# Performance work log

Hardware: AMD Instinct MI355X
Metric: run time of the kernel (lower is better)

The kernel has to match this reference:

```python
import jax, jax.numpy as jnp
import numpy as np

N_USER, N_ITEM, D, N_LAYER, NNZ, B = 50000, 100000, 64, 3, 2400000, 4096
NEG_SLOPE = 0.2
EPS = 1e-12


def setup_inputs() -> dict:
    key = jax.random.key(0)
    ks = jax.random.split(key, 12)
    N = N_USER + N_ITEM
    user_emb = jax.random.normal(ks[0], (N_USER, D), dtype=jnp.float32) * 0.1
    item_emb = jax.random.normal(ks[1], (N_ITEM, D), dtype=jnp.float32) * 0.1
    rows = jax.random.randint(ks[2], (NNZ,), 0, N, dtype=jnp.int32)
    cols = jax.random.randint(ks[3], (NNZ,), 0, N, dtype=jnp.int32)
    edge_index = jnp.stack([rows, cols])  # [2, nnz] COO indices of sparse L
    # normalized-Laplacian-like positive values, ~1/deg scale
    edge_vals = jax.random.uniform(ks[4], (NNZ,), dtype=jnp.float32) * (1.0 / 16.0)
    scale = 1.0 / np.sqrt(D)
    W1 = jax.random.normal(ks[5], (N_LAYER, D, D), dtype=jnp.float32) * scale
    W2 = jax.random.normal(ks[6], (N_LAYER, D, D), dtype=jnp.float32) * scale
    b1 = jnp.zeros((N_LAYER, D), dtype=jnp.float32)
    b2 = jnp.zeros((N_LAYER, D), dtype=jnp.float32)
    users = jax.random.randint(ks[7], (B,), 1, N_USER + 1, dtype=jnp.int32)      # 1-indexed
    pos_items = jax.random.randint(ks[8], (B,), 1, N_ITEM + 1, dtype=jnp.int32)  # 1-indexed
    neg_items = jax.random.randint(ks[9], (B,), 1, N_ITEM + 1, dtype=jnp.int32)  # 1-indexed
    return {"user_emb": user_emb, "item_emb": item_emb, "edge_vals": edge_vals,
            "W1": W1, "b1": b1, "W2": W2, "b2": b2,
            "edge_index": edge_index, "users": users,
            "pos_items": pos_items, "neg_items": neg_items}


def _spmm(rows, cols, vals, E, num_nodes):
    # sparse COO L @ E : gather source rows, scale by edge value, scatter-add to dest rows
    return jax.ops.segment_sum(vals[:, None] * E[cols], rows, num_segments=num_nodes)


def reference(user_emb, item_emb, edge_vals, W1, b1, W2, b2,
              edge_index, users, pos_items, neg_items):
    n_user = user_emb.shape[0]
    N = n_user + item_emb.shape[0]
    rows, cols = edge_index[0], edge_index[1]
    E = jnp.concatenate([user_emb, item_emb], axis=0)  # [N, d]
    all_E = [E]
    for i in range(W1.shape[0]):
        LE = _spmm(rows, cols, edge_vals, E, N)          # L @ E
        # (L + I) @ E @ W1 + (L@E * E) @ W2  (dropouts are eval-mode identity)
        h = (LE + E) @ W1[i] + b1[i] + (LE * E) @ W2[i] + b2[i]
        E = jax.nn.leaky_relu(h, NEG_SLOPE)
        nrm = jnp.maximum(jnp.linalg.norm(E, axis=1, keepdims=True), EPS)
        all_E.append(E / nrm)  # L2-normalized copy stored; unnormalized E propagates
    all_E = jnp.concatenate(all_E, axis=1)               # [N, d*(1+L)]
    u_emb = all_E[:n_user][users - 1]
    items = all_E[n_user:]
    return u_emb, items[pos_items - 1], items[neg_items - 1]
```

## Files before the change

### kernel.cpp

```cpp
#include <hip/hip_runtime.h>

#define N_USERC 50000
#define N_ITEMC 100000
#define NN      150000
#define DD      64
#define NLAYER  3
#define NNZC    2400000
#define BB      4096
#define NRID    (3*BB)
#define NBKT    147
#define NABLK   586
#define NTILE   4688
#define ELLW    32
#define ELLROWS 150528
#define OVCAP   32768

typedef unsigned short ushort_t;
typedef __attribute__((ext_vector_type(8))) short bf16x8;
typedef __attribute__((ext_vector_type(4))) float f32x4;

static __device__ __forceinline__ float bf2f(ushort_t b) {
    unsigned int u = ((unsigned int)b) << 16;
    return __uint_as_float(u);
}
static __device__ __forceinline__ ushort_t f2bf(float f) {
    unsigned int u = __float_as_uint(f);
    u = u + 0x7FFFu + ((u >> 16) & 1u);
    return (ushort_t)(u >> 16);
}

__global__ __launch_bounds__(256) void k_sniffzb(const unsigned int* __restrict__ ue_words,
                                                 int* __restrict__ flag,
                                                 int* __restrict__ bucket_cnt,
                                                 int* __restrict__ ovcnt) {
    int t = threadIdx.x;
    if (t < 64) {
        int cnt = 0;
        for (int i = 0; i < 4; i++) {
            unsigned int w = ue_words[t * 4 + i];
            unsigned int lo = w & 0xFFFFu;
            unsigned int ex = (lo >> 7) & 0xFF;
            if (ex >= 100 && ex <= 132) cnt++;
        }
        for (int m = 1; m < 64; m <<= 1) cnt += __shfl_xor(cnt, m, 64);
        if (t == 0) *flag = (cnt >= 128) ? 1 : 0;
    } else if (t - 64 < NBKT) {
        bucket_cnt[t - 64] = 0;
    } else if (t == 255) {
        *ovcnt = 0;
    }
}

__global__ __launch_bounds__(256) void k_initb(const void* __restrict__ ue,
                                               const void* __restrict__ ie,
                                               const int* __restrict__ flag,
                                               ushort_t* __restrict__ Eb0) {
    int i4 = blockIdx.x * 256 + threadIdx.x;
    if (i4 >= NN * DD / 4) return;
    int idx = i4 * 4;
    int row = idx >> 6;
    bool isU = row < N_USERC;
    int si = isU ? idx : idx - N_USERC * DD;
    if (*flag) {
        const uint2* src = (const uint2*)((const ushort_t*)(isU ? ue : ie) + si);
        *(uint2*)(Eb0 + idx) = *src;
    } else {
        const float* src = (const float*)(isU ? ue : ie) + si;
        ushort_t o[4];
#pragma unroll
        for (int k = 0; k < 4; k++) o[k] = f2bf(src[k]);
        *(uint2*)(Eb0 + idx) = *(uint2*)o;
    }
}

__global__ __launch_bounds__(256) void k_wprep(const void* __restrict__ W1,
                                               const void* __restrict__ W2,
                                               const void* __restrict__ b1,
                                               const void* __restrict__ b2,
                                               const int* __restrict__ flag,
                                               ushort_t* __restrict__ Wfrag,
                                               float* __restrict__ bsum) {
    int idx = blockIdx.x * 256 + threadIdx.x;
    int isbf = *flag;
    if (idx < NLAYER * 4 * 4 * 64 * 8) {
        int i    = idx & 7;
        int lane = (idx >> 3) & 63;
        int jt   = (idx >> 9) & 3;
        int s    = (idx >> 11) & 3;
        int l    = idx >> 13;
        int kfull = 32 * (s & 1) + 8 * (lane >> 4) + i;
        int col   = jt * 16 + (lane & 15);
        const void* W = (s < 2) ? W1 : W2;
        size_t off = (size_t)l * 4096 + (size_t)kfull * 64 + col;
        float v = isbf ? bf2f(((const ushort_t*)W)[off]) : ((const float*)W)[off];
        Wfrag[idx] = f2bf(v);
    } else {
        int r = idx - NLAYER * 4 * 4 * 64 * 8;
        if (r < NLAYER * 64) {
            float v1 = isbf ? bf2f(((const ushort_t*)b1)[r]) : ((const float*)b1)[r];
            float v2 = isbf ? bf2f(((const ushort_t*)b2)[r]) : ((const float*)b2)[r];
            bsum[r] = v1 + v2;
        }
    }
}

__global__ __launch_bounds__(256) void k_bhist(const int* __restrict__ rows,
                                               int* __restrict__ bucket_cnt) {
    __shared__ int h[NBKT];
    int t = threadIdx.x;
    if (t < NBKT) h[t] = 0;
    __syncthreads();
    int e0 = blockIdx.x * 4096;
#pragma unroll
    for (int i = 0; i < 16; i++) {
        int e = e0 + t + i * 256;
        if (e < NNZC) atomicAdd(&h[rows[e] >> 10], 1);
    }
    __syncthreads();
    if (t < NBKT && h[t]) atomicAdd(&bucket_cnt[t], h[t]);
}

__global__ __launch_bounds__(256) void k_bscan(const int* __restrict__ bucket_cnt,
                                               int* __restrict__ gbase,
                                               int* __restrict__ gcursor) {
    __shared__ int s[256];
    int t = threadIdx.x;
    int v = (t < NBKT) ? bucket_cnt[t] : 0;
    s[t] = v; __syncthreads();
    for (int off = 1; off < 256; off <<= 1) {
        int x = (t >= off) ? s[t - off] : 0;
        __syncthreads();
        s[t] += x;
        __syncthreads();
    }
    if (t < NBKT) { int ex = s[t] - v; gbase[t] = ex; gcursor[t] = ex; }
    if (t == 0) { gbase[NBKT] = NNZC; }
}

__global__ __launch_bounds__(256) void k_phaseA(const int* __restrict__ rows,
                                                const int* __restrict__ cols,
                                                const void* __restrict__ vals,
                                                const int* __restrict__ flag,
                                                int* __restrict__ gcursor,
                                                int2* __restrict__ binned) {
    __shared__ int hist[NBKT], base_[NBKT], lcur[NBKT];
    int t = threadIdx.x;
    int e0 = blockIdx.x * 4096;
    if (t < NBKT) { hist[t] = 0; lcur[t] = 0; }
    __syncthreads();
    int myrow[16];
#pragma unroll
    for (int i = 0; i < 16; i++) {
        int e = e0 + t + i * 256;
        int r = -1;
        if (e < NNZC) { r = rows[e]; atomicAdd(&hist[r >> 10], 1); }
        myrow[i] = r;
    }
    __syncthreads();
    if (t < NBKT && hist[t] > 0) base_[t] = atomicAdd(&gcursor[t], hist[t]);
    __syncthreads();
    int isbf = *flag;
#pragma unroll
    for (int i = 0; i < 16; i++) {
        int e = e0 + t + i * 256;
        if (e < NNZC) {
            int r = myrow[i];
            int bkt = r >> 10;
            int off = atomicAdd(&lcur[bkt], 1);
            int pos = base_[bkt] + off;
            int c = cols[e];
            float v = isbf ? bf2f(((const ushort_t*)vals)[e]) : ((const float*)vals)[e];
            binned[pos] = make_int2(((r & 1023) << 18) | c, __float_as_int(v));
        }
    }
}

__global__ __launch_bounds__(256) void k_phaseB(const int* __restrict__ gbase,
                                                const int2* __restrict__ binned,
                                                int2* __restrict__ ell,
                                                int4* __restrict__ ovbuf,
                                                int* __restrict__ ovcnt) {
    __shared__ int rcur[1024];
    int b = blockIdx.x, t = threadIdx.x;
    int s = gbase[b], e = gbase[b + 1];
    for (int i = t; i < 1024; i += 256) rcur[i] = 0;
    __syncthreads();
    for (int i = s + t; i < e; i += 256) {
        int2 en = binned[i];
        int rl = en.x >> 18;
        int c  = en.x & 0x3FFFF;
        int off = atomicAdd(&rcur[rl], 1);
        if (off < ELLW) {
            ell[((size_t)(b * 1024 + rl)) * ELLW + off] = make_int2(c, en.y);
        } else {
            int p = atomicAdd(ovcnt, 1);
            if (p < OVCAP) ovbuf[p] = make_int4(b * 1024 + rl, c, en.y, 0);
        }
    }
    __syncthreads();
    for (int i = t; i < 1024; i += 256) {
        int start = rcur[i]; if (start > ELLW) start = ELLW;
        int2* rp = ell + ((size_t)(b * 1024 + i)) * ELLW;
        for (int j = start; j < ELLW; j++) rp[j] = make_int2(0, 0);
    }
}

__global__ __launch_bounds__(256) void k_layer(const int2* __restrict__ ell,
                                               const int4* __restrict__ ovbuf,
                                               const int* __restrict__ ovcnt,
                                               const ushort_t* __restrict__ Eb_in,
                                               ushort_t* __restrict__ Eb_out,
                                               const ushort_t* __restrict__ Wfrag,
                                               const float* __restrict__ bsum,
                                               int layer) {
    __shared__ float sLE[32][68];
    __shared__ float sE [32][68];

    int t    = threadIdx.x;
    int wv   = t >> 6;
    int lane = t & 63;
    int oct  = lane >> 3;
    int d8   = (lane & 7) * 8;
    int hl   = lane >> 4;
    int l16  = lane & 15;
    int r0   = blockIdx.x << 5;

    int lr_ = t >> 3;
    int dm_ = (t & 7) * 8;
    uint4 ev = make_uint4(0u, 0u, 0u, 0u);
    {
        int gr = r0 + lr_;
        if (gr < NN) ev = *(const uint4*)(Eb_in + (size_t)gr * DD + dm_);
    }

    int baseRow = r0 + wv * 8;
    int2 pv_c[4], pv_n[4];
    uint4 q_c[4];
#pragma unroll
    for (int v = 0; v < 4; v++)
        pv_c[v] = ell[(size_t)baseRow * ELLW + v * 8 + oct];
#pragma unroll
    for (int v = 0; v < 4; v++)
        q_c[v] = *(const uint4*)(Eb_in + ((size_t)(unsigned)pv_c[v].x << 6) + d8);
#pragma unroll
    for (int v = 0; v < 4; v++)
        pv_n[v] = ell[(size_t)(baseRow + 1) * ELLW + v * 8 + oct];

#pragma unroll
    for (int sub = 0; sub < 8; sub++) {
        uint4 q_n[4];
        int2 pv_n2[4];
        if (sub < 7) {
#pragma unroll
            for (int v = 0; v < 4; v++)
                q_n[v] = *(const uint4*)(Eb_in + ((size_t)(unsigned)pv_n[v].x << 6) + d8);
        }
        if (sub < 6) {
#pragma unroll
            for (int v = 0; v < 4; v++)
                pv_n2[v] = ell[(size_t)(baseRow + sub + 2) * ELLW + v * 8 + oct];
        }
        float acc[8];
#pragma unroll
        for (int k = 0; k < 8; k++) acc[k] = 0.f;
#pragma unroll
        for (int v = 0; v < 4; v++) {
            float w = __int_as_float(pv_c[v].y);
            acc[0] = fmaf(w, __uint_as_float(q_c[v].x << 16),         acc[0]);
            acc[1] = fmaf(w, __uint_as_float(q_c[v].x & 0xffff0000u), acc[1]);
            acc[2] = fmaf(w, __uint_as_float(q_c[v].y << 16),         acc[2]);
            acc[3] = fmaf(w, __uint_as_float(q_c[v].y & 0xffff0000u), acc[3]);
            acc[4] = fmaf(w, __uint_as_float(q_c[v].z << 16),         acc[4]);
            acc[5] = fmaf(w, __uint_as_float(q_c[v].z & 0xffff0000u), acc[5]);
            acc[6] = fmaf(w, __uint_as_float(q_c[v].w << 16),         acc[6]);
            acc[7] = fmaf(w, __uint_as_float(q_c[v].w & 0xffff0000u), acc[7]);
        }
#pragma unroll
        for (int m = 8; m < 64; m <<= 1)
#pragma unroll
            for (int k = 0; k < 8; k++) acc[k] += __shfl_xor(acc[k], m, 64);
        if (oct == 0) {
            int lr = wv * 8 + sub;
            *(float4*)&sLE[lr][d8]     = make_float4(acc[0], acc[1], acc[2], acc[3]);
            *(float4*)&sLE[lr][d8 + 4] = make_float4(acc[4], acc[5], acc[6], acc[7]);
        }
#pragma unroll
        for (int v = 0; v < 4; v++) {
            pv_c[v] = pv_n[v];
            q_c[v]  = q_n[v];
            pv_n[v] = pv_n2[v];
        }
    }

    sE[lr_][dm_ + 0] = __uint_as_float(ev.x << 16);
    sE[lr_][dm_ + 1] = __uint_as_float(ev.x & 0xffff0000u);
    sE[lr_][dm_ + 2] = __uint_as_float(ev.y << 16);
    sE[lr_][dm_ + 3] = __uint_as_float(ev.y & 0xffff0000u);
    sE[lr_][dm_ + 4] = __uint_as_float(ev.z << 16);
    sE[lr_][dm_ + 5] = __uint_as_float(ev.z & 0xffff0000u);
    sE[lr_][dm_ + 6] = __uint_as_float(ev.w << 16);
    sE[lr_][dm_ + 7] = __uint_as_float(ev.w & 0xffff0000u);
    __syncthreads();

    {
        int n = *ovcnt;
        n = (n < OVCAP) ? n : OVCAP;
        if (wv == 0) {
            for (int i = 0; i < n; i++) {
                int4 ov = ovbuf[i];
                if ((unsigned)(ov.x - r0) < 32u) {
                    float w = __int_as_float(ov.z);
                    sLE[ov.x - r0][lane] += w * bf2f(Eb_in[(size_t)ov.y * DD + lane]);
                }
            }
        }
    }
    __syncthreads();

    int rt = wv & 1;
    int j0w = wv >> 1;
    int jtA = 2 * j0w, jtB = 2 * j0w + 1;
    const uint4* wb = (const uint4*)(Wfrag + (size_t)layer * 8192);
    float bsA = bsum[layer * 64 + jtA * 16 + l16];
    float bsB = bsum[layer * 64 + jtB * 16 + l16];

    f32x4 accA = (f32x4){0.f, 0.f, 0.f, 0.f};
    f32x4 accB = (f32x4){0.f, 0.f, 0.f, 0.f};
    int lrow = rt * 16 + l16;

#pragma unroll
    for (int sh = 0; sh < 2; sh++) {
        bf16x8 w1a, w1b, w2a, w2b;
        {
            uint4 qa = wb[(sh * 4 + jtA) * 64 + lane];
            uint4 qb = wb[(sh * 4 + jtB) * 64 + lane];
            uint4 qc = wb[((2 + sh) * 4 + jtA) * 64 + lane];
            uint4 qd = wb[((2 + sh) * 4 + jtB) * 64 + lane];
            __builtin_memcpy(&w1a, &qa, 16);
            __builtin_memcpy(&w1b, &qb, 16);
            __builtin_memcpy(&w2a, &qc, 16);
            __builtin_memcpy(&w2b, &qd, 16);
        }
        const float* pl = &sLE[lrow][sh * 32 + hl * 8];
        const float* pe = &sE [lrow][sh * 32 + hl * 8];
        float4 l0 = *(const float4*)pl, l1 = *(const float4*)(pl + 4);
        float4 e0 = *(const float4*)pe, e1 = *(const float4*)(pe + 4);
        float le[8] = {l0.x, l0.y, l0.z, l0.w, l1.x, l1.y, l1.z, l1.w};
        float ee[8] = {e0.x, e0.y, e0.z, e0.w, e1.x, e1.y, e1.z, e1.w};
        unsigned int u1h[4], u1l[4], u2h[4], u2l[4];
#pragma unroll
        for (int d = 0; d < 4; d++) {
            float s0 = le[2*d]   + ee[2*d];
            float s1 = le[2*d+1] + ee[2*d+1];
            float m0 = le[2*d]   * ee[2*d];
            float m1 = le[2*d+1] * ee[2*d+1];
            asm("v_cvt_pk_bf16_f32 %0, %1, %2" : "=v"(u1h[d]) : "v"(s0), "v"(s1));
            asm("v_cvt_pk_bf16_f32 %0, %1, %2" : "=v"(u2h[d]) : "v"(m0), "v"(m1));
            float s0r = s0 - __uint_as_float(u1h[d] << 16);
            float s1r = s1 - __uint_as_float(u1h[d] & 0xffff0000u);
            float m0r = m0 - __uint_as_float(u2h[d] << 16);
            float m1r = m1 - __uint_as_float(u2h[d] & 0xffff0000u);
            asm("v_cvt_pk_bf16_f32 %0, %1, %2" : "=v"(u1l[d]) : "v"(s0r), "v"(s1r));
            asm("v_cvt_pk_bf16_f32 %0, %1, %2" : "=v"(u2l[d]) : "v"(m0r), "v"(m1r));
        }
        bf16x8 p1h, p1l, p2h, p2l;
        __builtin_memcpy(&p1h, u1h, 16);
        __builtin_memcpy(&p1l, u1l, 16);
        __builtin_memcpy(&p2h, u2h, 16);
        __builtin_memcpy(&p2l, u2l, 16);

        accA = __builtin_amdgcn_mfma_f32_16x16x32_bf16(p1h, w1a, accA, 0, 0, 0);
        accA = __builtin_amdgcn_mfma_f32_16x16x32_bf16(p1l, w1a, accA, 0, 0, 0);
        accA = __builtin_amdgcn_mfma_f32_16x16x32_bf16(p2h, w2a, accA, 0, 0, 0);
        accA = __builtin_amdgcn_mfma_f32_16x16x32_bf16(p2l, w2a, accA, 0, 0, 0);
        accB = __builtin_amdgcn_mfma_f32_16x16x32_bf16(p1h, w1b, accB, 0, 0, 0);
        accB = __builtin_amdgcn_mfma_f32_16x16x32_bf16(p1l, w1b, accB, 0, 0, 0);
        accB = __builtin_amdgcn_mfma_f32_16x16x32_bf16(p2h, w2b, accB, 0, 0, 0);
        accB = __builtin_amdgcn_mfma_f32_16x16x32_bf16(p2l, w2b, accB, 0, 0, 0);
    }

#pragma unroll
    for (int g = 0; g < 4; g++) {
        int r = r0 + rt * 16 + hl * 4 + g;
        if (r < NN) {
            float hA = accA[g] + bsA; hA = (hA >= 0.f) ? hA : 0.2f * hA;
            float hB = accB[g] + bsB; hB = (hB >= 0.f) ? hB : 0.2f * hB;
            Eb_out[(size_t)r * DD + jtA * 16 + l16] = f2bf(hA);
            Eb_out[(size_t)r * DD + jtB * 16 + l16] = f2bf(hB);
        }
    }
}

static __device__ __forceinline__ int rid_to_node(int rid,
                                                  const int* users, const int* pos, const int* neg) {
    if (rid < BB)      return users[rid] - 1;
    if (rid < 2 * BB)  return N_USERC + pos[rid - BB] - 1;
    return N_USERC + neg[rid - 2 * BB] - 1;
}

__global__ __launch_bounds__(256) void k_outslice0(const ushort_t* __restrict__ Eb,
                                                   const int* __restrict__ users,
                                                   const int* __restrict__ pos,
                                                   const int* __restrict__ neg,
                                                   float* __restrict__ out) {
    int rid  = blockIdx.x * 4 + (threadIdx.x >> 6);
    int lane = threadIdx.x & 63;
    if (rid >= NRID) return;
    int node = rid_to_node(rid, users, pos, neg);
    out[(size_t)rid * 256 + lane] = bf2f(Eb[(size_t)node * DD + lane]);
}

__global__ __launch_bounds__(256) void k_outnorm(const ushort_t* __restrict__ Eb,
                                                 const int* __restrict__ users,
                                                 const int* __restrict__ pos,
                                                 const int* __restrict__ neg,
                                                 float* __restrict__ out,
                                                 int cbase) {
    int rid  = blockIdx.x * 4 + (threadIdx.x >> 6);
    int lane = threadIdx.x & 63;
    if (rid >= NRID) return;
    int node = rid_to_node(rid, users, pos, neg);
    float v = bf2f(Eb[(size_t)node * DD + lane]);
    float p2 = v * v;
    for (int m = 1; m < 64; m <<= 1) p2 += __shfl_xor(p2, m, 64);
    float nr = fmaxf(sqrtf(p2), 1e-12f);
    out[(size_t)rid * 256 + cbase + lane] = v / nr;
}

extern "C" void kernel_launch(void* const* d_in, const int* in_sizes, int n_in,
                              void* d_out, int out_size, void* d_ws, size_t ws_size,
                              hipStream_t stream) {
    const void* ue   = d_in[0];
    const void* ie   = d_in[1];
    const void* ev   = d_in[2];
    const void* W1   = d_in[3];
    const void* b1   = d_in[4];
    const void* W2   = d_in[5];
    const void* b2   = d_in[6];
    const int*  ei   = (const int*)d_in[7];
    const int*  usr  = (const int*)d_in[8];
    const int*  posi = (const int*)d_in[9];
    const int*  negi = (const int*)d_in[10];
    float*      out  = (float*)d_out;

    const int* rows = ei;
    const int* cols = ei + NNZC;

    char* w = (char*)d_ws;
    ushort_t* Eb1     = (ushort_t*)w; w += (size_t)NN * DD * 2;
    int2*   binned    = (int2*)w;   w += (size_t)NNZC * 8;
    ushort_t* Eb0     = (ushort_t*)binned;
    int2*   ell       = (int2*)w;   w += (size_t)ELLROWS * ELLW * 8;
    int4*   ovbuf     = (int4*)w;   w += (size_t)OVCAP * 16;
    int*    ovcnt     = (int*)w;    w += 256;
    int*    gbase     = (int*)w;    w += 1024;
    int*    gcursor   = (int*)w;    w += 1024;
    int*    bucket_cnt= (int*)w;    w += 1024;
    int*    flag      = (int*)w;    w += 256;
    ushort_t* Wfrag   = (ushort_t*)w; w += 49152;
    float*  bsum      = (float*)w;  w += 768;

    k_sniffzb<<<1, 256, 0, stream>>>((const unsigned int*)ue, flag, bucket_cnt, ovcnt);
    k_wprep<<<97, 256, 0, stream>>>(W1, W2, b1, b2, flag, Wfrag, bsum);
    k_bhist<<<NABLK, 256, 0, stream>>>(rows, bucket_cnt);
    k_bscan<<<1, 256, 0, stream>>>(bucket_cnt, gbase, gcursor);
    k_phaseA<<<NABLK, 256, 0, stream>>>(rows, cols, ev, flag, gcursor, binned);
    k_phaseB<<<NBKT, 256, 0, stream>>>(gbase, binned, ell, ovbuf, ovcnt);
    k_initb<<<9375, 256, 0, stream>>>(ue, ie, flag, Eb0);

    k_outslice0<<<3072, 256, 0, stream>>>(Eb0, usr, posi, negi, out);

    for (int l = 0; l < NLAYER; l++) {
        const ushort_t* ebi = (l & 1) ? Eb1 : Eb0;
        ushort_t*       ebo = (l & 1) ? Eb0 : Eb1;
        k_layer<<<NTILE, 256, 0, stream>>>(ell, ovbuf, ovcnt, ebi, ebo, Wfrag, bsum, l);
        k_outnorm<<<3072, 256, 0, stream>>>(ebo, usr, posi, negi, out, 64 * (l + 1));
    }
}
```

Baseline: 424.8 us.

## Build ELL directly with per-row atomics and fuse preprocessing launches

Replaces the bucketed two-pass COO-to-ELL build (histogram, scan, binning, per-bucket scatter) with one pass that zero-fills the ELL, row counters and overflow counter, then scatters each edge using a global per-row atomic counter. Weight prep is folded into the same kernel, and embedding conversion is merged with the layer-0 output slice, so seven setup launches become three. The single-pass build trades the staging writes and reads of the binned array for many global atomics and scattered writes plus an explicit memset of the whole ELL. Edge order within rows becomes nondeterministic.

Measured after the change: 519.4 us. +22.3%, slower.

```diff
diff --git a/kernel.cpp b/kernel.cpp
--- a/kernel.cpp
+++ b/kernel.cpp
@@ -8,12 +8,21 @@
 #define NNZC    2400000
 #define BB      4096
 #define NRID    (3*BB)
-#define NBKT    147
-#define NABLK   586
 #define NTILE   4688
 #define ELLW    32
 #define ELLROWS 150528
 #define OVCAP   32768
+#define NEBLK   586
+#define NWPB    97
+#define NPREPB  (NWPB + NEBLK)
+#define NIB     9375
+#define NOSB    3072
+#define NISB    (NIB + NOSB)
+#define ELL4    2408448
+#define RC4     37632
+#define OV4     64
+#define NZ4     (ELL4 + RC4 + OV4)
+#define NZB     9556
 
 typedef unsigned short ushort_t;
 typedef __attribute__((ext_vector_type(8))) short bf16x8;
@@ -29,12 +38,13 @@
     return (ushort_t)(u >> 16);
 }
 
-__global__ __launch_bounds__(256) void k_sniffzb(const unsigned int* __restrict__ ue_words,
-                                                 int* __restrict__ flag,
-                                                 int* __restrict__ bucket_cnt,
-                                                 int* __restrict__ ovcnt) {
-    int t = threadIdx.x;
-    if (t < 64) {
+__global__ __launch_bounds__(256) void k_sniffz(const unsigned int* __restrict__ ue_words,
+                                                int* __restrict__ flag,
+                                                int4* __restrict__ zbase) {
+    int idx = blockIdx.x * 256 + threadIdx.x;
+    if (idx < NZ4) zbase[idx] = make_int4(0, 0, 0, 0);
+    if (blockIdx.x == 0 && threadIdx.x < 64) {
+        int t = threadIdx.x;
         int cnt = 0;
         for (int i = 0; i < 4; i++) {
             unsigned int w = ue_words[t * 4 + i];
@@ -44,164 +54,110 @@
         }
         for (int m = 1; m < 64; m <<= 1) cnt += __shfl_xor(cnt, m, 64);
         if (t == 0) *flag = (cnt >= 128) ? 1 : 0;
-    } else if (t - 64 < NBKT) {
-        bucket_cnt[t - 64] = 0;
-    } else if (t == 255) {
-        *ovcnt = 0;
-    }
-}
-
-__global__ __launch_bounds__(256) void k_initb(const void* __restrict__ ue,
-                                               const void* __restrict__ ie,
-                                               const int* __restrict__ flag,
-                                               ushort_t* __restrict__ Eb0) {
-    int i4 = blockIdx.x * 256 + threadIdx.x;
-    if (i4 >= NN * DD / 4) return;
-    int idx = i4 * 4;
-    int row = idx >> 6;
-    bool isU = row < N_USERC;
-    int si = isU ? idx : idx - N_USERC * DD;
-    if (*flag) {
-        const uint2* src = (const uint2*)((const ushort_t*)(isU ? ue : ie) + si);
-        *(uint2*)(Eb0 + idx) = *src;
+    }
+}
+
+__global__ __launch_bounds__(256) void k_prep(const void* __restrict__ W1,
+                                              const void* __restrict__ W2,
+                                              const void* __restrict__ b1,
+                                              const void* __restrict__ b2,
+                                              const int* __restrict__ rows,
+                                              const int* __restrict__ cols,
+                                              const void* __restrict__ vals,
+                                              const int* __restrict__ flag,
+                                              ushort_t* __restrict__ Wfrag,
+                                              float* __restrict__ bsum,
+                                              int* __restrict__ rowcnt,
+                                              int2* __restrict__ ell,
+                                              int4* __restrict__ ovbuf,
+                                              int* __restrict__ ovcnt) {
+    int isbf = *flag;
+    if (blockIdx.x < NWPB) {
+        int idx = blockIdx.x * 256 + threadIdx.x;
+        if (idx < NLAYER * 4 * 4 * 64 * 8) {
+            int i    = idx & 7;
+            int lane = (idx >> 3) & 63;
+            int jt   = (idx >> 9) & 3;
+            int s    = (idx >> 11) & 3;
+            int l    = idx >> 13;
+            int kfull = 32 * (s & 1) + 8 * (lane >> 4) + i;
+            int col   = jt * 16 + (lane & 15);
+            const void* W = (s < 2) ? W1 : W2;
+            size_t off = (size_t)l * 4096 + (size_t)kfull * 64 + col;
+            float v = isbf ? bf2f(((const ushort_t*)W)[off]) : ((const float*)W)[off];
+            Wfrag[idx] = f2bf(v);
+        } else {
+            int r = idx - NLAYER * 4 * 4 * 64 * 8;
+            if (r < NLAYER * 64) {
+                float v1 = isbf ? bf2f(((const ushort_t*)b1)[r]) : ((const float*)b1)[r];
+                float v2 = isbf ? bf2f(((const ushort_t*)b2)[r]) : ((const float*)b2)[r];
+                bsum[r] = v1 + v2;
+            }
+        }
     } else {
-        const float* src = (const float*)(isU ? ue : ie) + si;
-        ushort_t o[4];
-#pragma unroll
-        for (int k = 0; k < 4; k++) o[k] = f2bf(src[k]);
-        *(uint2*)(Eb0 + idx) = *(uint2*)o;
-    }
-}
-
-__global__ __launch_bounds__(256) void k_wprep(const void* __restrict__ W1,
-                                               const void* __restrict__ W2,
-                                               const void* __restrict__ b1,
-                                               const void* __restrict__ b2,
-                                               const int* __restrict__ flag,
-                                               ushort_t* __restrict__ Wfrag,
-                                               float* __restrict__ bsum) {
-    int idx = blockIdx.x * 256 + threadIdx.x;
-    int isbf = *flag;
-    if (idx < NLAYER * 4 * 4 * 64 * 8) {
-        int i    = idx & 7;
-        int lane = (idx >> 3) & 63;
-        int jt   = (idx >> 9) & 3;
-        int s    = (idx >> 11) & 3;
-        int l    = idx >> 13;
-        int kfull = 32 * (s & 1) + 8 * (lane >> 4) + i;
-        int col   = jt * 16 + (lane & 15);
-        const void* W = (s < 2) ? W1 : W2;
-        size_t off = (size_t)l * 4096 + (size_t)kfull * 64 + col;
-        float v = isbf ? bf2f(((const ushort_t*)W)[off]) : ((const float*)W)[off];
-        Wfrag[idx] = f2bf(v);
+        int e0 = (blockIdx.x - NWPB) * 4096;
+        int t = threadIdx.x;
+#pragma unroll
+        for (int i = 0; i < 16; i++) {
+            int e = e0 + t + i * 256;
+            if (e < NNZC) {
+                int r = rows[e];
+                int c = cols[e];
+                float v = isbf ? bf2f(((const ushort_t*)vals)[e]) : ((const float*)vals)[e];
+                int off = atomicAdd(&rowcnt[r], 1);
+                if (off < ELLW) {
+                    ell[(size_t)r * ELLW + off] = make_int2(c, __float_as_int(v));
+                } else {
+                    int p = atomicAdd(ovcnt, 1);
+                    if (p < OVCAP) ovbuf[p] = make_int4(r, c, __float_as_int(v), 0);
+                }
+            }
+        }
+    }
+}
+
+static __device__ __forceinline__ int rid_to_node(int rid,
+                                                  const int* users, const int* pos, const int* neg) {
+    if (rid < BB)      return users[rid] - 1;
+    if (rid < 2 * BB)  return N_USERC + pos[rid - BB] - 1;
+    return N_USERC + neg[rid - 2 * BB] - 1;
+}
+
+__global__ __launch_bounds__(256) void k_initslice(const void* __restrict__ ue,
+                                                   const void* __restrict__ ie,
+                                                   const int* __restrict__ flag,
+                                                   ushort_t* __restrict__ Eb0,
+                                                   const int* __restrict__ users,
+                                                   const int* __restrict__ pos,
+                                                   const int* __restrict__ neg,
+                                                   float* __restrict__ out) {
+    if (blockIdx.x < NIB) {
+        int i4 = blockIdx.x * 256 + threadIdx.x;
+        if (i4 >= NN * DD / 4) return;
+        int idx = i4 * 4;
+        int row = idx >> 6;
+        bool isU = row < N_USERC;
+        int si = isU ? idx : idx - N_USERC * DD;
+        if (*flag) {
+            const uint2* src = (const uint2*)((const ushort_t*)(isU ? ue : ie) + si);
+            *(uint2*)(Eb0 + idx) = *src;
+        } else {
+            const float* src = (const float*)(isU ? ue : ie) + si;
+            ushort_t o[4];
+#pragma unroll
+            for (int k = 0; k < 4; k++) o[k] = f2bf(src[k]);
+            *(uint2*)(Eb0 + idx) = *(uint2*)o;
+        }
     } else {
-        int r = idx - NLAYER * 4 * 4 * 64 * 8;
-        if (r < NLAYER * 64) {
-            float v1 = isbf ? bf2f(((const ushort_t*)b1)[r]) : ((const float*)b1)[r];
-            float v2 = isbf ? bf2f(((const ushort_t*)b2)[r]) : ((const float*)b2)[r];
-            bsum[r] = v1 + v2;
-        }
-    }
-}
-
-__global__ __launch_bounds__(256) void k_bhist(const int* __restrict__ rows,
-                                               int* __restrict__ bucket_cnt) {
-    __shared__ int h[NBKT];
-    int t = threadIdx.x;
-    if (t < NBKT) h[t] = 0;
-    __syncthreads();
-    int e0 = blockIdx.x * 4096;
-#pragma unroll
-    for (int i = 0; i < 16; i++) {
-        int e = e0 + t + i * 256;
-        if (e < NNZC) atomicAdd(&h[rows[e] >> 10], 1);
-    }
-    __syncthreads();
-    if (t < NBKT && h[t]) atomicAdd(&bucket_cnt[t], h[t]);
-}
-
-__global__ __launch_bounds__(256) void k_bscan(const int* __restrict__ bucket_cnt,
-                                               int* __restrict__ gbase,
-                                               int* __restrict__ gcursor) {
-    __shared__ int s[256];
-    int t = threadIdx.x;
-    int v = (t < NBKT) ? bucket_cnt[t] : 0;
-    s[t] = v; __syncthreads();
-    for (int off = 1; off < 256; off <<= 1) {
-        int x = (t >= off) ? s[t - off] : 0;
-        __syncthreads();
-        s[t] += x;
-        __syncthreads();
-    }
-    if (t < NBKT) { int ex = s[t] - v; gbase[t] = ex; gcursor[t] = ex; }
-    if (t == 0) { gbase[NBKT] = NNZC; }
-}
-
-__global__ __launch_bounds__(256) void k_phaseA(const int* __restrict__ rows,
-                                                const int* __restrict__ cols,
-                                                const void* __restrict__ vals,
-                                                const int* __restrict__ flag,
-                                                int* __restrict__ gcursor,
-                                                int2* __restrict__ binned) {
-    __shared__ int hist[NBKT], base_[NBKT], lcur[NBKT];
-    int t = threadIdx.x;
-    int e0 = blockIdx.x * 4096;
-    if (t < NBKT) { hist[t] = 0; lcur[t] = 0; }
-    __syncthreads();
-    int myrow[16];
-#pragma unroll
-    for (int i = 0; i < 16; i++) {
-        int e = e0 + t + i * 256;
-        int r = -1;
-        if (e < NNZC) { r = rows[e]; atomicAdd(&hist[r >> 10], 1); }
-        myrow[i] = r;
-    }
-    __syncthreads();
-    if (t < NBKT && hist[t] > 0) base_[t] = atomicAdd(&gcursor[t], hist[t]);
-    __syncthreads();
-    int isbf = *flag;
-#pragma unroll
-    for (int i = 0; i < 16; i++) {
-        int e = e0 + t + i * 256;
-        if (e < NNZC) {
-            int r = myrow[i];
-            int bkt = r >> 10;
-            int off = atomicAdd(&lcur[bkt], 1);
-            int pos = base_[bkt] + off;
-            int c = cols[e];
-            float v = isbf ? bf2f(((const ushort_t*)vals)[e]) : ((const float*)vals)[e];
-            binned[pos] = make_int2(((r & 1023) << 18) | c, __float_as_int(v));
-        }
-    }
-}
-
-__global__ __launch_bounds__(256) void k_phaseB(const int* __restrict__ gbase,
-                                                const int2* __restrict__ binned,
-                                                int2* __restrict__ ell,
-                                                int4* __restrict__ ovbuf,
-                                                int* __restrict__ ovcnt) {
-    __shared__ int rcur[1024];
-    int b = blockIdx.x, t = threadIdx.x;
-    int s = gbase[b], e = gbase[b + 1];
-    for (int i = t; i < 1024; i += 256) rcur[i] = 0;
-    __syncthreads();
-    for (int i = s + t; i < e; i += 256) {
-        int2 en = binned[i];
-        int rl = en.x >> 18;
-        int c  = en.x & 0x3FFFF;
-        int off = atomicAdd(&rcur[rl], 1);
-        if (off < ELLW) {
-            ell[((size_t)(b * 1024 + rl)) * ELLW + off] = make_int2(c, en.y);
-        } else {
-            int p = atomicAdd(ovcnt, 1);
-            if (p < OVCAP) ovbuf[p] = make_int4(b * 1024 + rl, c, en.y, 0);
-        }
-    }
-    __syncthreads();
-    for (int i = t; i < 1024; i += 256) {
-        int start = rcur[i]; if (start > ELLW) start = ELLW;
-        int2* rp = ell + ((size_t)(b * 1024 + i)) * ELLW;
-        for (int j = start; j < ELLW; j++) rp[j] = make_int2(0, 0);
+        int rid  = (blockIdx.x - NIB) * 4 + (threadIdx.x >> 6);
+        int lane = threadIdx.x & 63;
+        if (rid >= NRID) return;
+        int node = rid_to_node(rid, users, pos, neg);
+        bool isU = node < N_USERC;
+        int si = (isU ? node : node - N_USERC) * DD + lane;
+        float v = (*flag) ? bf2f(isU ? ((const ushort_t*)ue)[si] : ((const ushort_t*)ie)[si])
+                          : (isU ? ((const float*)ue)[si] : ((const float*)ie)[si]);
+        out[(size_t)rid * 256 + lane] = v;
     }
 }
 
@@ -389,25 +345,6 @@
             Eb_out[(size_t)r * DD + jtB * 16 + l16] = f2bf(hB);
         }
     }
-}
-
-static __device__ __forceinline__ int rid_to_node(int rid,
-                                                  const int* users, const int* pos, const int* neg) {
-    if (rid < BB)      return users[rid] - 1;
-    if (rid < 2 * BB)  return N_USERC + pos[rid - BB] - 1;
-    return N_USERC + neg[rid - 2 * BB] - 1;
-}
-
-__global__ __launch_bounds__(256) void k_outslice0(const ushort_t* __restrict__ Eb,
-                                                   const int* __restrict__ users,
-                                                   const int* __restrict__ pos,
-                                                   const int* __restrict__ neg,
-                                                   float* __restrict__ out) {
-    int rid  = blockIdx.x * 4 + (threadIdx.x >> 6);
-    int lane = threadIdx.x & 63;
-    if (rid >= NRID) return;
-    int node = rid_to_node(rid, users, pos, neg);
-    out[(size_t)rid * 256 + lane] = bf2f(Eb[(size_t)node * DD + lane]);
 }
 
 __global__ __launch_bounds__(256) void k_outnorm(const ushort_t* __restrict__ Eb,
@@ -448,27 +385,19 @@
 
     char* w = (char*)d_ws;
     ushort_t* Eb1     = (ushort_t*)w; w += (size_t)NN * DD * 2;
-    int2*   binned    = (int2*)w;   w += (size_t)NNZC * 8;
-    ushort_t* Eb0     = (ushort_t*)binned;
+    ushort_t* Eb0     = (ushort_t*)w; w += (size_t)NN * DD * 2;
     int2*   ell       = (int2*)w;   w += (size_t)ELLROWS * ELLW * 8;
+    int*    rowcnt    = (int*)w;    w += (size_t)ELLROWS * 4;
+    int*    ovcnt     = (int*)w;    w += 1024;
     int4*   ovbuf     = (int4*)w;   w += (size_t)OVCAP * 16;
-    int*    ovcnt     = (int*)w;    w += 256;
-    int*    gbase     = (int*)w;    w += 1024;
-    int*    gcursor   = (int*)w;    w += 1024;
-    int*    bucket_cnt= (int*)w;    w += 1024;
     int*    flag      = (int*)w;    w += 256;
     ushort_t* Wfrag   = (ushort_t*)w; w += 49152;
     float*  bsum      = (float*)w;  w += 768;
 
-    k_sniffzb<<<1, 256, 0, stream>>>((const unsigned int*)ue, flag, bucket_cnt, ovcnt);
-    k_wprep<<<97, 256, 0, stream>>>(W1, W2, b1, b2, flag, Wfrag, bsum);
-    k_bhist<<<NABLK, 256, 0, stream>>>(rows, bucket_cnt);
-    k_bscan<<<1, 256, 0, stream>>>(bucket_cnt, gbase, gcursor);
-    k_phaseA<<<NABLK, 256, 0, stream>>>(rows, cols, ev, flag, gcursor, binned);
-    k_phaseB<<<NBKT, 256, 0, stream>>>(gbase, binned, ell, ovbuf, ovcnt);
-    k_initb<<<9375, 256, 0, stream>>>(ue, ie, flag, Eb0);
-
-    k_outslice0<<<3072, 256, 0, stream>>>(Eb0, usr, posi, negi, out);
+    k_sniffz<<<NZB, 256, 0, stream>>>((const unsigned int*)ue, flag, (int4*)ell);
+    k_prep<<<NPREPB, 256, 0, stream>>>(W1, W2, b1, b2, rows, cols, ev, flag,
+                                       Wfrag, bsum, rowcnt, ell, ovbuf, ovcnt);
+    k_initslice<<<NISB, 256, 0, stream>>>(ue, ie, flag, Eb0, usr, posi, negi, out);
 
     for (int l = 0; l < NLAYER; l++) {
         const ushort_t* ebi = (l & 1) ? Eb1 : Eb0;
```
